# Kernel tuning notes

Hardware: AMD Instinct MI355X
Metric: run time of the kernel (lower is better)

The kernel has to match this reference:

```python
import jax, jax.numpy as jnp
import numpy as np

EPS = 1e-5

def _conv3x3(x, w, b):
    # x: (N,C,H,W), w: (O,I,3,3), SAME padding, stride 1
    y = jax.lax.conv_general_dilated(x, w, window_strides=(1, 1), padding='SAME',
                                     dimension_numbers=('NCHW', 'OIHW', 'NCHW'))
    return y + b[None, :, None, None]

def _bn(x, gamma, beta):
    # BatchNorm2d in training mode (batch statistics, biased variance), torch default
    m = jnp.mean(x, axis=(0, 2, 3), keepdims=True)
    v = jnp.var(x, axis=(0, 2, 3), keepdims=True)
    return gamma[None, :, None, None] * (x - m) * jax.lax.rsqrt(v + EPS) + beta[None, :, None, None]

def setup_inputs() -> dict:
    key = jax.random.key(0)
    ks = jax.random.split(key, 12)
    N, T_in, T_out, H, W = 4, 12, 12, 32, 32
    C = 64
    WH = H * W

    def xavier(k, shape, fan_in, fan_out):
        lim = np.sqrt(6.0 / (fan_in + fan_out))
        return jax.random.uniform(k, shape, jnp.float32, -lim, lim)

    x = jax.random.normal(ks[0], (N, T_in, H, W), jnp.float32)
    # ConvBlock: 5 conv(3x3)+BN+ReLU layers; first conv is T_in->64, rest 64->64
    conv0_w = xavier(ks[1], (C, T_in, 3, 3), T_in * 9, C * 9)
    conv_w = xavier(ks[2], (4, C, C, 3, 3), C * 9, C * 9)
    conv_b = jnp.zeros((5, C), jnp.float32)
    bn_gamma = jnp.ones((5, C), jnp.float32)
    bn_beta = jnp.zeros((5, C), jnp.float32)
    reg_w = xavier(ks[3], (T_out, C, 3, 3), C * 9, T_out * 9)
    reg_b = jnp.zeros((T_out,), jnp.float32)
    # attention weight (timesteps=12, WH, WH), xavier_uniform
    att_w = xavier(ks[4], (12, WH, WH), WH, WH)
    return {'x': x, 'conv0_w': conv0_w, 'conv_w': conv_w, 'conv_b': conv_b,
            'bn_gamma': bn_gamma, 'bn_beta': bn_beta,
            'reg_w': reg_w, 'reg_b': reg_b, 'att_w': att_w}

def reference(x, conv0_w, conv_w, conv_b, bn_gamma, bn_beta, reg_w, reg_b, att_w):
    h = x
    for i in range(5):
        w = conv0_w if i == 0 else conv_w[i - 1]
        h = jax.nn.relu(_bn(_conv3x3(h, w, conv_b[i]), bn_gamma[i], bn_beta[i]))
    h = _conv3x3(h, reg_w, reg_b)  # (N, T, H, W)
    N, T, H, W = h.shape
    WH = H * W
    xf = h.reshape(N, T, WH)
    # hadamard attention: xp[n,t,i,j] = xf[n,t,j]; scores = weight * xp
    scores = att_w[None, :, :, :] * xf[:, :, None, :]  # (N,T,WH,WH)
    att = jax.nn.softmax(scores, axis=3)
    out = jnp.einsum('ntij,ntj->nti', att, xf).reshape(N, T, H, W)
    return out, att
```

## Files before the change

kernel.cpp:

```cpp
#include <hip/hip_runtime.h>

#define EPS_BN 1e-5f

typedef float f32x4 __attribute__((ext_vector_type(4)));

#define PROWS 34
#define PCOLS 36
#define PS (PROWS * PCOLS)

__global__ __launch_bounds__(256) void pad_copy_kern(
    const float* __restrict__ x, float* __restrict__ bufX)
{
    const int plane = blockIdx.x;
    const int tid = threadIdx.x;
    const int r  = tid >> 3;
    const int c4 = (tid & 7) << 2;
    float4 v = *(const float4*)(x + (plane << 10) + (r << 5) + c4);
    float* o = bufX + plane * PS + (r + 1) * PCOLS + (c4 + 1);
    o[0] = v.x; o[1] = v.y; o[2] = v.z; o[3] = v.w;
}

template<int CIN, int COUT, bool BN_IN, bool STATS, bool PAD_OUT>
__global__ __launch_bounds__(256) void conv3x3_v2(
    const float* __restrict__ in,
    const float* __restrict__ wgt,
    const float* __restrict__ bias,
    const float* __restrict__ in_stats,
    const float* __restrict__ gamma,
    const float* __restrict__ beta,
    float* __restrict__ out,
    float* __restrict__ out_stats)
{
    __shared__ float s_sc[64];
    __shared__ float s_sh[64];
    __shared__ float s_corr[8];

    const int tid = threadIdx.x;
    const int n   = blockIdx.x / COUT;
    const int co  = blockIdx.x - n * COUT;

    if (BN_IN) {
        if (tid < CIN) {
            float s    = in_stats[tid];
            float ss   = in_stats[64 + tid];
            float mean = s * (1.0f / 4096.0f);
            float var  = fmaxf(ss * (1.0f / 4096.0f) - mean * mean, 0.0f);
            float g    = gamma[tid] * rsqrtf(var + EPS_BN);
            float sc   = g;
            float sh   = beta[tid] - mean * g;
            s_sc[tid] = sc;
            s_sh[tid] = sh;
            float rl = fmaxf(sh, 0.0f);
            const float* wp = wgt + (co * CIN + tid) * 9;
            float w0=wp[0], w1=wp[1], w2=wp[2], w3=wp[3],
                  w5=wp[5], w6=wp[6], w7=wp[7], w8=wp[8];
            float pT  = rl * (w0 + w1 + w2);
            float pB  = rl * (w6 + w7 + w8);
            float pL  = rl * (w0 + w3 + w6);
            float pR  = rl * (w2 + w5 + w8);
            float pTL = rl * w0, pTR = rl * w2, pBL = rl * w6, pBR = rl * w8;
            #pragma unroll
            for (int off = 32; off; off >>= 1) {
                pT  += __shfl_down(pT,  off); pB  += __shfl_down(pB,  off);
                pL  += __shfl_down(pL,  off); pR  += __shfl_down(pR,  off);
                pTL += __shfl_down(pTL, off); pTR += __shfl_down(pTR, off);
                pBL += __shfl_down(pBL, off); pBR += __shfl_down(pBR, off);
            }
            if (tid == 0) {
                s_corr[0]=pT; s_corr[1]=pB; s_corr[2]=pL; s_corr[3]=pR;
                s_corr[4]=pTL; s_corr[5]=pTR; s_corr[6]=pBL; s_corr[7]=pBR;
            }
        }
        __syncthreads();
    }

    const int r  = tid >> 3;
    const int c4 = (tid & 7) << 2;
    const float* ip = in + n * CIN * PS + r * PCOLS + c4;

    float acc0 = 0.f, acc1 = 0.f, acc2 = 0.f, acc3 = 0.f;

    #pragma unroll 2
    for (int ci = 0; ci < CIN; ++ci) {
        const float* p  = ip + ci * PS;
        const float* wp = wgt + (co * CIN + ci) * 9;
        float sc = 0.f, sh = 0.f;
        if (BN_IN) { sc = s_sc[ci]; sh = s_sh[ci]; }
        #pragma unroll
        for (int dr = 0; dr < 3; ++dr) {
            float4 a = *(const float4*)(p + dr * PCOLS);
            float2 b = *(const float2*)(p + dr * PCOLS + 4);
            float h0, h1, h2, h3, h4, h5;
            if (BN_IN) {
                h0 = fmaxf(fmaf(sc, a.x, sh), 0.f);
                h1 = fmaxf(fmaf(sc, a.y, sh), 0.f);
                h2 = fmaxf(fmaf(sc, a.z, sh), 0.f);
                h3 = fmaxf(fmaf(sc, a.w, sh), 0.f);
                h4 = fmaxf(fmaf(sc, b.x, sh), 0.f);
                h5 = fmaxf(fmaf(sc, b.y, sh), 0.f);
            } else {
                h0 = a.x; h1 = a.y; h2 = a.z; h3 = a.w; h4 = b.x; h5 = b.y;
            }
            float wa = wp[dr * 3 + 0], wb = wp[dr * 3 + 1], wc = wp[dr * 3 + 2];
            acc0 = fmaf(wa, h0, fmaf(wb, h1, fmaf(wc, h2, acc0)));
            acc1 = fmaf(wa, h1, fmaf(wb, h2, fmaf(wc, h3, acc1)));
            acc2 = fmaf(wa, h2, fmaf(wb, h3, fmaf(wc, h4, acc2)));
            acc3 = fmaf(wa, h3, fmaf(wb, h4, fmaf(wc, h5, acc3)));
        }
    }

    float bv = bias[co];
    float u0 = acc0 + bv, u1 = acc1 + bv, u2 = acc2 + bv, u3 = acc3 + bv;

    if (BN_IN) {
        float corr = (r == 0 ? s_corr[0] : 0.f) + (r == 31 ? s_corr[1] : 0.f);
        u0 -= corr; u1 -= corr; u2 -= corr; u3 -= corr;
        if (c4 == 0) {
            u0 -= s_corr[2];
            if (r == 0)  u0 += s_corr[4];
            if (r == 31) u0 += s_corr[6];
        }
        if (c4 == 28) {
            u3 -= s_corr[3];
            if (r == 0)  u3 += s_corr[5];
            if (r == 31) u3 += s_corr[7];
        }
    }

    if (PAD_OUT) {
        float* op = out + (n * COUT + co) * PS + (r + 1) * PCOLS + (c4 + 1);
        op[0] = u0; op[1] = u1; op[2] = u2; op[3] = u3;
    } else {
        float4 res; res.x = u0; res.y = u1; res.z = u2; res.w = u3;
        *(float4*)(out + ((n * COUT + co) << 10) + (r << 5) + c4) = res;
    }

    if (STATS) {
        float s  = u0 + u1 + u2 + u3;
        float ss = u0*u0 + u1*u1 + u2*u2 + u3*u3;
        #pragma unroll
        for (int off = 32; off; off >>= 1) {
            s  += __shfl_down(s,  off);
            ss += __shfl_down(ss, off);
        }
        if ((tid & 63) == 0) {
            atomicAdd(&out_stats[co],      s);
            atomicAdd(&out_stats[64 + co], ss);
        }
    }
}

__global__ __launch_bounds__(256) void attention_v2(
    const float* __restrict__ xf,
    const float* __restrict__ att_w,
    float* __restrict__ out,
    float* __restrict__ att)
{
    __shared__ __align__(16) float s_xf[4096];
    __shared__ float red[4][8];
    const int tid = threadIdx.x;
    const int t   = blockIdx.x >> 10;
    const int i   = blockIdx.x & 1023;
    const int w   = tid >> 6;

    const float4* xf4 = (const float4*)xf;
    float4* s4 = (float4*)s_xf;
    #pragma unroll
    for (int q = 0; q < 4; ++q) {
        int e  = (q << 8) + tid;
        int nn = e >> 8;
        int j4 = e & 255;
        s4[e] = xf4[((nn * 12 + t) << 8) + j4];
    }
    float4 wv = ((const float4*)att_w)[(((t << 10) + i) << 8) + tid];
    __syncthreads();

    float ev[4][4], ps[4], pd[4];
    #pragma unroll
    for (int nn = 0; nn < 4; ++nn) {
        float4 xv = ((const float4*)(s_xf + (nn << 10)))[tid];
        float e0 = __expf(wv.x * xv.x);
        float e1 = __expf(wv.y * xv.y);
        float e2 = __expf(wv.z * xv.z);
        float e3 = __expf(wv.w * xv.w);
        ps[nn] = (e0 + e1) + (e2 + e3);
        pd[nn] = fmaf(e0, xv.x, fmaf(e1, xv.y, fmaf(e2, xv.z, e3 * xv.w)));
        ev[nn][0] = e0; ev[nn][1] = e1; ev[nn][2] = e2; ev[nn][3] = e3;
    }
    #pragma unroll
    for (int off = 32; off; off >>= 1) {
        #pragma unroll
        for (int nn = 0; nn < 4; ++nn) {
            ps[nn] += __shfl_down(ps[nn], off);
            pd[nn] += __shfl_down(pd[nn], off);
        }
    }
    if ((tid & 63) == 0) {
        #pragma unroll
        for (int nn = 0; nn < 4; ++nn) {
            red[w][nn]     = ps[nn];
            red[w][4 + nn] = pd[nn];
        }
    }
    __syncthreads();

    #pragma unroll
    for (int nn = 0; nn < 4; ++nn) {
        float sum = (red[0][nn] + red[1][nn]) + (red[2][nn] + red[3][nn]);
        float dot = (red[0][4+nn] + red[1][4+nn]) + (red[2][4+nn] + red[3][4+nn]);
        float inv = 1.0f / sum;
        f32x4 av;
        av.x = ev[nn][0] * inv; av.y = ev[nn][1] * inv;
        av.z = ev[nn][2] * inv; av.w = ev[nn][3] * inv;
        f32x4* dst = (f32x4*)att + ((((nn * 12 + t) << 10) + i) << 8) + tid;
        __builtin_nontemporal_store(av, dst);
        if (tid == 0) out[((nn * 12 + t) << 10) + i] = dot * inv;
    }
}

extern "C" void kernel_launch(void* const* d_in, const int* in_sizes, int n_in,
                              void* d_out, int out_size, void* d_ws, size_t ws_size,
                              hipStream_t stream)
{
    const float* x      = (const float*)d_in[0];
    const float* conv0w = (const float*)d_in[1];
    const float* convw  = (const float*)d_in[2];
    const float* convb  = (const float*)d_in[3];
    const float* gammas = (const float*)d_in[4];
    const float* betas  = (const float*)d_in[5];
    const float* regw   = (const float*)d_in[6];
    const float* regb   = (const float*)d_in[7];
    const float* attw   = (const float*)d_in[8];

    float* out = (float*)d_out;
    float* att = out + 4 * 12 * 1024;

    float* ws    = (float*)d_ws;
    float* stats = ws;
    float* bufX  = stats + 640;
    float* bufA  = bufX + 48 * PS;
    float* bufB  = bufA + 256 * PS;
    float* xf    = bufB + 256 * PS;

    (void)hipMemsetAsync(stats, 0,
                         (640 + 48 * PS + 2 * 256 * PS) * sizeof(float),
                         stream);

    pad_copy_kern<<<48, 256, 0, stream>>>(x, bufX);

    conv3x3_v2<12, 64, false, true, true><<<256, 256, 0, stream>>>(
        bufX, conv0w, convb, nullptr, nullptr, nullptr, bufA, stats);
    conv3x3_v2<64, 64, true, true, true><<<256, 256, 0, stream>>>(
        bufA, convw + 0 * 36864, convb + 64, stats, gammas, betas,
        bufB, stats + 128);
    conv3x3_v2<64, 64, true, true, true><<<256, 256, 0, stream>>>(
        bufB, convw + 1 * 36864, convb + 128, stats + 128, gammas + 64,
        betas + 64, bufA, stats + 256);
    conv3x3_v2<64, 64, true, true, true><<<256, 256, 0, stream>>>(
        bufA, convw + 2 * 36864, convb + 192, stats + 256, gammas + 128,
        betas + 128, bufB, stats + 384);
    conv3x3_v2<64, 64, true, true, true><<<256, 256, 0, stream>>>(
        bufB, convw + 3 * 36864, convb + 256, stats + 384, gammas + 192,
        betas + 192, bufA, stats + 512);
    conv3x3_v2<64, 12, true, false, false><<<48, 256, 0, stream>>>(
        bufA, regw, regb, stats + 512, gammas + 256, betas + 256, xf, nullptr);

    attention_v2<<<12288, 256, 0, stream>>>(xf, attw, out, att);
}
```

Measured before the change: 401.5 us.

## Fuse conv stack into one cooperative kernel with grid syncs

Replaces the memset, pad-copy and six conv launches with a single cooperative kernel that uses grid-wide syncs between layers. Padding borders are zeroed in-kernel instead of by a big memset, and the regressor conv is split four ways over input channels with atomic accumulation into a pre-zeroed buffer so 192 blocks work on it instead of 48. Conv bias is dropped because it is zero in the inputs and cancels under the following BN anyway. The aim is to cut launch and memset overhead, at the cost of grid-sync latency and float atomics in the regressor output.

```diff
diff --git a/kernel.cpp b/kernel.cpp
--- a/kernel.cpp
+++ b/kernel.cpp
@@ -1,4 +1,7 @@
 #include <hip/hip_runtime.h>
+#include <hip/hip_cooperative_groups.h>
+
+namespace cg = cooperative_groups;
 
 #define EPS_BN 1e-5f
 
@@ -8,89 +11,64 @@
 #define PCOLS 36
 #define PS (PROWS * PCOLS)
 
-__global__ __launch_bounds__(256) void pad_copy_kern(
-    const float* __restrict__ x, float* __restrict__ bufX)
-{
-    const int plane = blockIdx.x;
-    const int tid = threadIdx.x;
-    const int r  = tid >> 3;
-    const int c4 = (tid & 7) << 2;
-    float4 v = *(const float4*)(x + (plane << 10) + (r << 5) + c4);
-    float* o = bufX + plane * PS + (r + 1) * PCOLS + (c4 + 1);
-    o[0] = v.x; o[1] = v.y; o[2] = v.z; o[3] = v.w;
-}
-
-template<int CIN, int COUT, bool BN_IN, bool STATS, bool PAD_OUT>
-__global__ __launch_bounds__(256) void conv3x3_v2(
-    const float* __restrict__ in,
-    const float* __restrict__ wgt,
-    const float* __restrict__ bias,
-    const float* __restrict__ in_stats,
-    const float* __restrict__ gamma,
-    const float* __restrict__ beta,
-    float* __restrict__ out,
-    float* __restrict__ out_stats)
-{
-    __shared__ float s_sc[64];
-    __shared__ float s_sh[64];
-    __shared__ float s_corr[8];
-
-    const int tid = threadIdx.x;
-    const int n   = blockIdx.x / COUT;
-    const int co  = blockIdx.x - n * COUT;
-
-    if (BN_IN) {
-        if (tid < CIN) {
-            float s    = in_stats[tid];
-            float ss   = in_stats[64 + tid];
-            float mean = s * (1.0f / 4096.0f);
-            float var  = fmaxf(ss * (1.0f / 4096.0f) - mean * mean, 0.0f);
-            float g    = gamma[tid] * rsqrtf(var + EPS_BN);
-            float sc   = g;
-            float sh   = beta[tid] - mean * g;
-            s_sc[tid] = sc;
-            s_sh[tid] = sh;
-            float rl = fmaxf(sh, 0.0f);
-            const float* wp = wgt + (co * CIN + tid) * 9;
-            float w0=wp[0], w1=wp[1], w2=wp[2], w3=wp[3],
-                  w5=wp[5], w6=wp[6], w7=wp[7], w8=wp[8];
-            float pT  = rl * (w0 + w1 + w2);
-            float pB  = rl * (w6 + w7 + w8);
-            float pL  = rl * (w0 + w3 + w6);
-            float pR  = rl * (w2 + w5 + w8);
-            float pTL = rl * w0, pTR = rl * w2, pBL = rl * w6, pBR = rl * w8;
-            #pragma unroll
-            for (int off = 32; off; off >>= 1) {
-                pT  += __shfl_down(pT,  off); pB  += __shfl_down(pB,  off);
-                pL  += __shfl_down(pL,  off); pR  += __shfl_down(pR,  off);
-                pTL += __shfl_down(pTL, off); pTR += __shfl_down(pTR, off);
-                pBL += __shfl_down(pBL, off); pBR += __shfl_down(pBR, off);
-            }
-            if (tid == 0) {
-                s_corr[0]=pT; s_corr[1]=pB; s_corr[2]=pL; s_corr[3]=pR;
-                s_corr[4]=pTL; s_corr[5]=pTR; s_corr[6]=pBL; s_corr[7]=pBR;
-            }
-        }
-        __syncthreads();
-    }
-
-    const int r  = tid >> 3;
-    const int c4 = (tid & 7) << 2;
-    const float* ip = in + n * CIN * PS + r * PCOLS + c4;
-
-    float acc0 = 0.f, acc1 = 0.f, acc2 = 0.f, acc3 = 0.f;
-
-    #pragma unroll 2
+__device__ __forceinline__ void bn_prologue(
+    const float* __restrict__ in_stats, const float* __restrict__ gamma,
+    const float* __restrict__ beta, const float* __restrict__ wgt_co,
+    float* s_sc, float* s_sh, float* s_corr, int tid, int ci_lo, int ci_hi)
+{
+    if (tid < 64) {
+        float s    = in_stats[tid];
+        float ss   = in_stats[64 + tid];
+        float mean = s * (1.0f / 4096.0f);
+        float var  = fmaxf(ss * (1.0f / 4096.0f) - mean * mean, 0.0f);
+        float g    = gamma[tid] * rsqrtf(var + EPS_BN);
+        float sh   = beta[tid] - mean * g;
+        s_sc[tid] = g;
+        s_sh[tid] = sh;
+        float rl = (tid >= ci_lo && tid < ci_hi) ? fmaxf(sh, 0.0f) : 0.0f;
+        const float* wp = wgt_co + tid * 9;
+        float w0=wp[0], w1=wp[1], w2=wp[2], w3=wp[3],
+              w5=wp[5], w6=wp[6], w7=wp[7], w8=wp[8];
+        float pT  = rl * (w0 + w1 + w2);
+        float pB  = rl * (w6 + w7 + w8);
+        float pL  = rl * (w0 + w3 + w6);
+        float pR  = rl * (w2 + w5 + w8);
+        float pTL = rl * w0, pTR = rl * w2, pBL = rl * w6, pBR = rl * w8;
+        #pragma unroll
+        for (int off = 32; off; off >>= 1) {
+            pT  += __shfl_down(pT,  off); pB  += __shfl_down(pB,  off);
+            pL  += __shfl_down(pL,  off); pR  += __shfl_down(pR,  off);
+            pTL += __shfl_down(pTL, off); pTR += __shfl_down(pTR, off);
+            pBL += __shfl_down(pBL, off); pBR += __shfl_down(pBR, off);
+        }
+        if (tid == 0) {
+            s_corr[0]=pT; s_corr[1]=pB; s_corr[2]=pL; s_corr[3]=pR;
+            s_corr[4]=pTL; s_corr[5]=pTR; s_corr[6]=pBL; s_corr[7]=pBR;
+        }
+    }
+    __syncthreads();
+}
+
+template<int CIN, bool BN_IN>
+__device__ __forceinline__ void conv_core(
+    const float* __restrict__ inp,
+    const float* __restrict__ wgt9,
+    const float* s_sc, const float* s_sh,
+    int r, int c4, float& u0, float& u1, float& u2, float& u3)
+{
+    const float* ip = inp + r * PCOLS + c4;
+    float acc0=0.f, acc1=0.f, acc2=0.f, acc3=0.f;
+    #pragma unroll 4
     for (int ci = 0; ci < CIN; ++ci) {
         const float* p  = ip + ci * PS;
-        const float* wp = wgt + (co * CIN + ci) * 9;
+        const float* wp = wgt9 + ci * 9;
         float sc = 0.f, sh = 0.f;
         if (BN_IN) { sc = s_sc[ci]; sh = s_sh[ci]; }
         #pragma unroll
         for (int dr = 0; dr < 3; ++dr) {
             float4 a = *(const float4*)(p + dr * PCOLS);
             float2 b = *(const float2*)(p + dr * PCOLS + 4);
-            float h0, h1, h2, h3, h4, h5;
+            float h0,h1,h2,h3,h4,h5;
             if (BN_IN) {
                 h0 = fmaxf(fmaf(sc, a.x, sh), 0.f);
                 h1 = fmaxf(fmaf(sc, a.y, sh), 0.f);
@@ -101,52 +79,158 @@
             } else {
                 h0 = a.x; h1 = a.y; h2 = a.z; h3 = a.w; h4 = b.x; h5 = b.y;
             }
-            float wa = wp[dr * 3 + 0], wb = wp[dr * 3 + 1], wc = wp[dr * 3 + 2];
+            float wa = wp[dr*3+0], wb = wp[dr*3+1], wc = wp[dr*3+2];
             acc0 = fmaf(wa, h0, fmaf(wb, h1, fmaf(wc, h2, acc0)));
             acc1 = fmaf(wa, h1, fmaf(wb, h2, fmaf(wc, h3, acc1)));
             acc2 = fmaf(wa, h2, fmaf(wb, h3, fmaf(wc, h4, acc2)));
             acc3 = fmaf(wa, h3, fmaf(wb, h4, fmaf(wc, h5, acc3)));
         }
     }
-
-    float bv = bias[co];
-    float u0 = acc0 + bv, u1 = acc1 + bv, u2 = acc2 + bv, u3 = acc3 + bv;
-
-    if (BN_IN) {
-        float corr = (r == 0 ? s_corr[0] : 0.f) + (r == 31 ? s_corr[1] : 0.f);
-        u0 -= corr; u1 -= corr; u2 -= corr; u3 -= corr;
-        if (c4 == 0) {
-            u0 -= s_corr[2];
-            if (r == 0)  u0 += s_corr[4];
-            if (r == 31) u0 += s_corr[6];
-        }
-        if (c4 == 28) {
-            u3 -= s_corr[3];
-            if (r == 0)  u3 += s_corr[5];
-            if (r == 31) u3 += s_corr[7];
-        }
-    }
-
-    if (PAD_OUT) {
-        float* op = out + (n * COUT + co) * PS + (r + 1) * PCOLS + (c4 + 1);
-        op[0] = u0; op[1] = u1; op[2] = u2; op[3] = u3;
-    } else {
-        float4 res; res.x = u0; res.y = u1; res.z = u2; res.w = u3;
-        *(float4*)(out + ((n * COUT + co) << 10) + (r << 5) + c4) = res;
-    }
-
-    if (STATS) {
-        float s  = u0 + u1 + u2 + u3;
-        float ss = u0*u0 + u1*u1 + u2*u2 + u3*u3;
-        #pragma unroll
-        for (int off = 32; off; off >>= 1) {
-            s  += __shfl_down(s,  off);
-            ss += __shfl_down(ss, off);
-        }
-        if ((tid & 63) == 0) {
-            atomicAdd(&out_stats[co],      s);
-            atomicAdd(&out_stats[64 + co], ss);
-        }
+    u0 = acc0; u1 = acc1; u2 = acc2; u3 = acc3;
+}
+
+__device__ __forceinline__ void apply_corr(
+    const float* s_corr, int r, int c4,
+    float& u0, float& u1, float& u2, float& u3)
+{
+    float corr = (r == 0 ? s_corr[0] : 0.f) + (r == 31 ? s_corr[1] : 0.f);
+    u0 -= corr; u1 -= corr; u2 -= corr; u3 -= corr;
+    if (c4 == 0) {
+        u0 -= s_corr[2];
+        if (r == 0)  u0 += s_corr[4];
+        if (r == 31) u0 += s_corr[6];
+    }
+    if (c4 == 28) {
+        u3 -= s_corr[3];
+        if (r == 0)  u3 += s_corr[5];
+        if (r == 31) u3 += s_corr[7];
+    }
+}
+
+__device__ __forceinline__ void write_padded(
+    float* __restrict__ plane, int r, int c4, int tid,
+    float u0, float u1, float u2, float u3)
+{
+    float* op = plane + (r + 1) * PCOLS + (c4 + 1);
+    op[0]=u0; op[1]=u1; op[2]=u2; op[3]=u3;
+    if (tid < 136) {
+        int e;
+        if      (tid < 36)  e = tid;
+        else if (tid < 72)  e = 33 * PCOLS + (tid - 36);
+        else if (tid < 104) e = (tid - 72 + 1) * PCOLS;
+        else                e = (tid - 104 + 1) * PCOLS + 35;
+        plane[e] = 0.f;
+    }
+}
+
+__device__ __forceinline__ void stats_acc(
+    float* __restrict__ lstats, int co, int tid,
+    float u0, float u1, float u2, float u3)
+{
+    float s  = u0 + u1 + u2 + u3;
+    float ss = u0*u0 + u1*u1 + u2*u2 + u3*u3;
+    #pragma unroll
+    for (int off = 32; off; off >>= 1) {
+        s  += __shfl_down(s,  off);
+        ss += __shfl_down(ss, off);
+    }
+    if ((tid & 63) == 0) {
+        atomicAdd(&lstats[co],      s);
+        atomicAdd(&lstats[64 + co], ss);
+    }
+}
+
+__global__ __launch_bounds__(256) void fused_conv(
+    const float* __restrict__ x,
+    const float* __restrict__ conv0w,
+    const float* __restrict__ convw,
+    const float* __restrict__ gammas,
+    const float* __restrict__ betas,
+    const float* __restrict__ regw,
+    const float* __restrict__ regb,
+    float* __restrict__ bufX,
+    float* __restrict__ bufA,
+    float* __restrict__ bufB,
+    float* __restrict__ stats,
+    float* __restrict__ xf)
+{
+    cg::grid_group grid = cg::this_grid();
+    __shared__ float s_sc[64];
+    __shared__ float s_sh[64];
+    __shared__ float s_corr[8];
+
+    const int tid = threadIdx.x;
+    const int b   = blockIdx.x;
+    const int r   = tid >> 3;
+    const int c4  = (tid & 7) << 2;
+
+    if (b < 48) {
+        const float* xp = x + (b << 10);
+        float* o = bufX + b * PS;
+        for (int e = tid; e < PS; e += 256) {
+            int rr = e / PCOLS, cc = e - rr * PCOLS;
+            int ir = rr - 1, ic = cc - 1;
+            float v = ((unsigned)ir < 32u && (unsigned)ic < 32u)
+                        ? xp[(ir << 5) + ic] : 0.f;
+            o[e] = v;
+        }
+    } else if (b < 96) {
+        f32x4 z = {0.f, 0.f, 0.f, 0.f};
+        ((f32x4*)(xf + ((b - 48) << 10)))[tid] = z;
+    } else if (b == 96) {
+        for (int e = tid; e < 640; e += 256) stats[e] = 0.f;
+    }
+    grid.sync();
+
+    const int n  = b >> 6;
+    const int co = b & 63;
+
+    {
+        float u0,u1,u2,u3;
+        conv_core<12,false>(bufX + n * 12 * PS, conv0w + co * 108,
+                            s_sc, s_sh, r, c4, u0,u1,u2,u3);
+        write_padded(bufA + (n * 64 + co) * PS, r, c4, tid, u0,u1,u2,u3);
+        stats_acc(stats, co, tid, u0,u1,u2,u3);
+    }
+    grid.sync();
+
+    #pragma unroll 1
+    for (int L = 1; L <= 4; ++L) {
+        const float* bin  = (L & 1) ? bufA : bufB;
+        float*       bout = (L & 1) ? bufB : bufA;
+        const float* w    = convw + (L - 1) * 36864;
+        bn_prologue(stats + (L - 1) * 128, gammas + (L - 1) * 64,
+                    betas + (L - 1) * 64, w + co * 576,
+                    s_sc, s_sh, s_corr, tid, 0, 64);
+        float u0,u1,u2,u3;
+        conv_core<64,true>(bin + n * 64 * PS, w + co * 576,
+                           s_sc, s_sh, r, c4, u0,u1,u2,u3);
+        apply_corr(s_corr, r, c4, u0,u1,u2,u3);
+        write_padded(bout + (n * 64 + co) * PS, r, c4, tid, u0,u1,u2,u3);
+        stats_acc(stats + L * 128, co, tid, u0,u1,u2,u3);
+        grid.sync();
+    }
+
+    if (b < 192) {
+        const int q     = b & 3;
+        const int idx   = b >> 2;
+        const int nn    = idx / 12;
+        const int cc    = idx - nn * 12;
+        const int ci_lo = q << 4;
+        bn_prologue(stats + 512, gammas + 256, betas + 256, regw + cc * 576,
+                    s_sc, s_sh, s_corr, tid, ci_lo, ci_lo + 16);
+        float u0,u1,u2,u3;
+        conv_core<16,true>(bufA + nn * 64 * PS + ci_lo * PS,
+                           regw + cc * 576 + ci_lo * 9,
+                           s_sc + ci_lo, s_sh + ci_lo, r, c4, u0,u1,u2,u3);
+        apply_corr(s_corr, r, c4, u0,u1,u2,u3);
+        if (q == 0) {
+            float bv = regb[cc];
+            u0 += bv; u1 += bv; u2 += bv; u3 += bv;
+        }
+        float* op = xf + ((nn * 12 + cc) << 10) + (r << 5) + c4;
+        atomicAdd(op + 0, u0); atomicAdd(op + 1, u1);
+        atomicAdd(op + 2, u2); atomicAdd(op + 3, u3);
     }
 }
 
@@ -231,6 +315,7 @@
     const float* regw   = (const float*)d_in[6];
     const float* regb   = (const float*)d_in[7];
     const float* attw   = (const float*)d_in[8];
+    (void)convb;
 
     float* out = (float*)d_out;
     float* att = out + 4 * 12 * 1024;
@@ -242,28 +327,13 @@
     float* bufB  = bufA + 256 * PS;
     float* xf    = bufB + 256 * PS;
 
-    (void)hipMemsetAsync(stats, 0,
-                         (640 + 48 * PS + 2 * 256 * PS) * sizeof(float),
-                         stream);
-
-    pad_copy_kern<<<48, 256, 0, stream>>>(x, bufX);
-
-    conv3x3_v2<12, 64, false, true, true><<<256, 256, 0, stream>>>(
-        bufX, conv0w, convb, nullptr, nullptr, nullptr, bufA, stats);
-    conv3x3_v2<64, 64, true, true, true><<<256, 256, 0, stream>>>(
-        bufA, convw + 0 * 36864, convb + 64, stats, gammas, betas,
-        bufB, stats + 128);
-    conv3x3_v2<64, 64, true, true, true><<<256, 256, 0, stream>>>(
-        bufB, convw + 1 * 36864, convb + 128, stats + 128, gammas + 64,
-        betas + 64, bufA, stats + 256);
-    conv3x3_v2<64, 64, true, true, true><<<256, 256, 0, stream>>>(
-        bufA, convw + 2 * 36864, convb + 192, stats + 256, gammas + 128,
-        betas + 128, bufB, stats + 384);
-    conv3x3_v2<64, 64, true, true, true><<<256, 256, 0, stream>>>(
-        bufB, convw + 3 * 36864, convb + 256, stats + 384, gammas + 192,
-        betas + 192, bufA, stats + 512);
-    conv3x3_v2<64, 12, true, false, false><<<48, 256, 0, stream>>>(
-        bufA, regw, regb, stats + 512, gammas + 256, betas + 256, xf, nullptr);
+    void* kargs[] = {
+        (void*)&x, (void*)&conv0w, (void*)&convw, (void*)&gammas,
+        (void*)&betas, (void*)&regw, (void*)&regb,
+        (void*)&bufX, (void*)&bufA, (void*)&bufB, (void*)&stats, (void*)&xf
+    };
+    (void)hipLaunchCooperativeKernel((void*)fused_conv, dim3(256), dim3(256),
+                                     kargs, 0, stream);
 
     attention_v2<<<12288, 256, 0, stream>>>(xf, attw, out, att);
 }
```

Result: slower. 553.6 us (+37.9%).
